# Kernel tuning notes

Hardware: AMD Instinct MI355X
Metric: run time of the kernel (lower is better)

## Reference

```python
import jax, jax.numpy as jnp
import numpy as np

N, E, IN, HID, OUT = 40000, 640000, 128, 512, 256


def setup_inputs() -> dict:
    key = jax.random.key(0)
    ks = jax.random.split(key, 8)
    x = jax.random.normal(ks[0], (N, IN), dtype=jnp.float32)
    edge_index = jax.random.randint(ks[1], (2, E), 0, N, dtype=jnp.int64)
    # SAGEConv params: lin_l (applied to aggregated neighbors, with bias),
    # lin_r (applied to root nodes, no bias) -- PyG defaults.
    def lin(k, fin, fout):
        return jax.random.normal(k, (fin, fout), dtype=jnp.float32) / np.sqrt(fin)
    return {
        "x": x,
        "edge_index": edge_index,
        "W1l": lin(ks[2], IN, HID),
        "b1": jnp.zeros((HID,), jnp.float32),
        "W1r": lin(ks[3], IN, HID),
        "W2l": lin(ks[4], HID, OUT),
        "b2": jnp.zeros((OUT,), jnp.float32),
        "W2r": lin(ks[5], HID, OUT),
    }


def _sage_conv(x, src, dst, Wl, b, Wr):
    n = x.shape[0]
    # gather messages from source nodes, mean-aggregate at destination
    msg = x[src]                                            # [E, F]
    agg = jax.ops.segment_sum(msg, dst, num_segments=n)     # [N, F]
    cnt = jax.ops.segment_sum(jnp.ones((src.shape[0],), x.dtype), dst,
                              num_segments=n)               # [N]
    agg = agg / jnp.maximum(cnt, 1.0)[:, None]
    # out = lin_l(mean_neighbors) + lin_r(x)
    return agg @ Wl + b + x @ Wr


def reference(x, edge_index, W1l, b1, W1r, W2l, b2, W2r):
    src, dst = edge_index[0], edge_index[1]
    h = jax.nn.relu(_sage_conv(x, src, dst, W1l, b1, W1r))
    return _sage_conv(h, src, dst, W2l, b2, W2r)
```

## Files before the change

### kernel.cpp

```cpp
#include <hip/hip_runtime.h>


#define N_NODES 40000
#define N_EDGES 640000
#define F_IN 128
#define F_HID 512
#define F_OUT 256
#define NB_SCAN 157

typedef unsigned short ushort_t;
typedef __attribute__((ext_vector_type(8))) short bf16x8;
typedef __attribute__((ext_vector_type(4))) float floatx4;

__device__ __forceinline__ ushort_t f2bf(float f) {
  union { float f; unsigned int u; } x; x.f = f;
  unsigned int r = (x.u + 0x7FFFu + ((x.u >> 16) & 1u)) >> 16;
  return (ushort_t)r;
}
__device__ __forceinline__ float bf2f(ushort_t u) {
  union { unsigned int u; float f; } x; x.u = ((unsigned int)u) << 16;
  return x.f;
}

__global__ void deg_kernel(const int* __restrict__ ei, int* __restrict__ deg) {
  int e = blockIdx.x * blockDim.x + threadIdx.x;
  if (e < N_EDGES) atomicAdd(&deg[ei[N_EDGES + e]], 1);
}

__global__ void scanA_kernel(const int* __restrict__ deg, int* __restrict__ bsum) {
  __shared__ int sdata[256];
  int i = blockIdx.x * 256 + threadIdx.x;
  sdata[threadIdx.x] = (i < N_NODES) ? deg[i] : 0;
  __syncthreads();
  #pragma unroll
  for (int off = 128; off > 0; off >>= 1) {
    if (threadIdx.x < off) sdata[threadIdx.x] += sdata[threadIdx.x + off];
    __syncthreads();
  }
  if (threadIdx.x == 0) bsum[blockIdx.x] = sdata[0];
}

__global__ void scanB_kernel(const int* __restrict__ bsum, int* __restrict__ boff) {
  __shared__ int buf[2][256];
  int tid = threadIdx.x;
  int v = (tid < NB_SCAN) ? bsum[tid] : 0;
  buf[0][tid] = v;
  __syncthreads();
  int cur = 0;
  #pragma unroll
  for (int off = 1; off < 256; off <<= 1) {
    int val = buf[cur][tid];
    if (tid >= off) val += buf[cur][tid - off];
    buf[cur ^ 1][tid] = val;
    __syncthreads();
    cur ^= 1;
  }
  if (tid < NB_SCAN) boff[tid] = buf[cur][tid] - v;
}

__global__ void scanC_kernel(const int* __restrict__ deg, const int* __restrict__ boff,
                             int* __restrict__ rowptr, int* __restrict__ cursor) {
  __shared__ int buf[2][256];
  int tid = threadIdx.x;
  int i = blockIdx.x * 256 + tid;
  int v = (i < N_NODES) ? deg[i] : 0;
  buf[0][tid] = v;
  __syncthreads();
  int cur = 0;
  #pragma unroll
  for (int off = 1; off < 256; off <<= 1) {
    int val = buf[cur][tid];
    if (tid >= off) val += buf[cur][tid - off];
    buf[cur ^ 1][tid] = val;
    __syncthreads();
    cur ^= 1;
  }
  if (i < N_NODES) {
    int ex = boff[blockIdx.x] + buf[cur][tid] - v;
    rowptr[i] = ex;
    cursor[i] = ex;
    if (i == N_NODES - 1) rowptr[N_NODES] = ex + v;
  }
}

__global__ void fill_kernel(const int* __restrict__ ei, int* __restrict__ cursor,
                            int* __restrict__ col) {
  int e = blockIdx.x * blockDim.x + threadIdx.x;
  if (e < N_EDGES) {
    int d = ei[N_EDGES + e];
    int s = ei[e];
    int pos = atomicAdd(&cursor[d], 1);
    col[pos] = s;
  }
}

__global__ void cvt_x_kernel(const float* __restrict__ x, ushort_t* __restrict__ xb) {
  int i = blockIdx.x * blockDim.x + threadIdx.x;
  const int n4 = (N_NODES * F_IN) / 4;
  if (i < n4) {
    float4 v = ((const float4*)x)[i];
    ushort4 o;
    o.x = f2bf(v.x); o.y = f2bf(v.y); o.z = f2bf(v.z); o.w = f2bf(v.w);
    ((ushort4*)xb)[i] = o;
  }
}

__global__ void wp_kernel(const float* __restrict__ W, ushort_t* __restrict__ Wp,
                          int K, int N, int rowoff, int koff, int KT) {
  int i = blockIdx.x * blockDim.x + threadIdx.x;
  if (i < K * N) {
    int n = i / K, k = i - n * K;
    int ng = rowoff + n, kg = koff + k;
    int gg = ng >> 6, ni = (ng >> 4) & 3, lm = ng & 15;
    int c = kg >> 3, j = kg & 7, t = c >> 2, qk = c & 3;
    size_t dst = (((size_t)(gg * (KT / 32) + t) * 4 + ni) * 64 + qk * 16 + lm) * 8 + j;
    Wp[dst] = f2bf(W[(size_t)k * N + n]);
  }
}

__global__ void biascat_kernel(const float* __restrict__ b2, float* __restrict__ bc) {
  int i = threadIdx.x + blockIdx.x * blockDim.x;
  if (i < 512) bc[i] = (i < 256) ? 0.f : b2[i - 256];
}

__global__ void agg1_kernel(const ushort_t* __restrict__ Xb, ushort_t* __restrict__ Yb,
                            const int* __restrict__ rowptr, const int* __restrict__ colidx) {
  __shared__ int cols[64];
  int n = blockIdx.x, f = threadIdx.x;
  int s = rowptr[n], e = rowptr[n + 1];
  float s0 = 0.f, s1 = 0.f;
  for (int base = s; base < e; base += 64) {
    int cnt = min(64, e - base);
    __syncthreads();
    if (f < cnt) cols[f] = colidx[base + f];
    __syncthreads();
    int j = 0;
    for (; j + 8 <= cnt; j += 8) {
      unsigned int v[8];
      #pragma unroll
      for (int u = 0; u < 8; ++u)
        v[u] = *(const unsigned int*)(Xb + (size_t)cols[j + u] * F_IN + 2 * f);
      #pragma unroll
      for (int u = 0; u < 8; ++u) {
        s0 += bf2f((ushort_t)(v[u] & 0xffffu));
        s1 += bf2f((ushort_t)(v[u] >> 16));
      }
    }
    for (; j < cnt; ++j) {
      unsigned int v = *(const unsigned int*)(Xb + (size_t)cols[j] * F_IN + 2 * f);
      s0 += bf2f((ushort_t)(v & 0xffffu));
      s1 += bf2f((ushort_t)(v >> 16));
    }
  }
  float inv = 1.f / fmaxf((float)(e - s), 1.f);
  unsigned int o = (unsigned int)f2bf(s0 * inv) | ((unsigned int)f2bf(s1 * inv) << 16);
  *(unsigned int*)(Yb + (size_t)n * F_IN + 2 * f) = o;
}

__global__ void agg2_kernel(const ushort_t* __restrict__ hl, const float* __restrict__ hr,
                            float* __restrict__ out,
                            const int* __restrict__ rowptr, const int* __restrict__ colidx) {
  __shared__ int cols[128];
  int n = blockIdx.x, f = threadIdx.x;
  int s = rowptr[n], e = rowptr[n + 1];
  float2 hrv = *(const float2*)(hr + (size_t)n * F_OUT + 2 * f);
  float s0 = 0.f, s1 = 0.f;
  for (int base = s; base < e; base += 128) {
    int cnt = min(128, e - base);
    __syncthreads();
    if (f < cnt) cols[f] = colidx[base + f];
    __syncthreads();
    int j = 0;
    for (; j + 8 <= cnt; j += 8) {
      unsigned int v[8];
      #pragma unroll
      for (int u = 0; u < 8; ++u)
        v[u] = *(const unsigned int*)(hl + (size_t)cols[j + u] * F_OUT + 2 * f);
      #pragma unroll
      for (int u = 0; u < 8; ++u) {
        s0 += bf2f((ushort_t)(v[u] & 0xffffu));
        s1 += bf2f((ushort_t)(v[u] >> 16));
      }
    }
    for (; j < cnt; ++j) {
      unsigned int v = *(const unsigned int*)(hl + (size_t)cols[j] * F_OUT + 2 * f);
      s0 += bf2f((ushort_t)(v & 0xffffu));
      s1 += bf2f((ushort_t)(v >> 16));
    }
  }
  float inv = 1.f / fmaxf((float)(e - s), 1.f);
  float2 o;
  o.x = s0 * inv + hrv.x;
  o.y = s1 * inv + hrv.y;
  *(float2*)(out + (size_t)n * F_OUT + 2 * f) = o;
}

template <bool TWOPAIR, bool RELU, bool BIAS, bool OUT_BF16, bool SPLITOUT, int KT>
__global__ __launch_bounds__(256) void gemm_mfma(
    const ushort_t* __restrict__ A0, const ushort_t* __restrict__ A1,
    const ushort_t* __restrict__ Wp, const float* __restrict__ bias,
    float* __restrict__ Cf, ushort_t* __restrict__ Cb, int M) {
  const int KH = (KT > 256) ? 256 : KT;
  const int NH = KT / KH;
  const int NKH = KH / 8;
  __shared__ ushort_t Apan[64 * KH];
  const int tid = threadIdx.x;
  const int wave = tid >> 6, lane = tid & 63;
  const int lm = lane & 15, qk = lane >> 4;
  const int bn = blockIdx.x * 256;
  const int bm = blockIdx.y * 64;
  const int K0 = TWOPAIR ? KT / 2 : KT;
  const int K0c = K0 / 8;

  const ushort_t* wpg = Wp + (size_t)(blockIdx.x * 4 + wave) * (KT / 32) * 2048;

  auto stageA = [&](int h) {
    #pragma unroll
    for (int q = 0; q < (64 * NKH) / 256; ++q) {
      int c = tid + q * 256;
      int lc = c & (NKH - 1);
      int row = c / NKH;
      int kc = h * NKH + lc;
      const ushort_t* src = (TWOPAIR && kc >= K0c)
          ? A1 + (size_t)(bm + row) * K0 + (kc - K0c) * 8
          : A0 + (size_t)(bm + row) * K0 + kc * 8;
      bf16x8 v = *(const bf16x8*)src;
      size_t off = ((size_t)(lc * 64 + row) * 16) ^ (size_t)((lc & 7) << 4);
      *(bf16x8*)((char*)Apan + off) = v;
    }
  };

  stageA(0);
  bf16x8 bvA[4], bvB[4];
  #pragma unroll
  for (int ni = 0; ni < 4; ++ni)
    bvA[ni] = *(const bf16x8*)(wpg + (size_t)ni * 512 + lane * 8);
  __syncthreads();

  floatx4 acc[4][4] = {};
  #pragma unroll 1
  for (int h = 0; h < NH; ++h) {
    if (h) {
      __syncthreads();
      stageA(h);
      __syncthreads();
    }
    #pragma unroll 1
    for (int kb = 0; kb < KH; kb += 64) {
      const int t0 = (h * KH + kb) / 32;
      #pragma unroll
      for (int ni = 0; ni < 4; ++ni)
        bvB[ni] = *(const bf16x8*)(wpg + ((size_t)(t0 + 1) * 4 + ni) * 512 + lane * 8);

      bf16x8 av[4];
      const int kc0 = kb / 8 + qk;
      #pragma unroll
      for (int mi = 0; mi < 4; ++mi) {
        size_t off = ((size_t)(kc0 * 64 + mi * 16 + lm) * 16) ^ (size_t)((kc0 & 7) << 4);
        av[mi] = *(const bf16x8*)((char*)Apan + off);
      }
      #pragma unroll
      for (int mi = 0; mi < 4; ++mi)
        #pragma unroll
        for (int ni = 0; ni < 4; ++ni)
          acc[mi][ni] = __builtin_amdgcn_mfma_f32_16x16x32_bf16(
              bvA[ni], av[mi], acc[mi][ni], 0, 0, 0);

      if (h * KH + kb + 64 < KT) {
        #pragma unroll
        for (int ni = 0; ni < 4; ++ni)
          bvA[ni] = *(const bf16x8*)(wpg + ((size_t)(t0 + 2) * 4 + ni) * 512 + lane * 8);
      }

      const int kc1 = kb / 8 + 4 + qk;
      #pragma unroll
      for (int mi = 0; mi < 4; ++mi) {
        size_t off = ((size_t)(kc1 * 64 + mi * 16 + lm) * 16) ^ (size_t)((kc1 & 7) << 4);
        av[mi] = *(const bf16x8*)((char*)Apan + off);
      }
      #pragma unroll
      for (int mi = 0; mi < 4; ++mi)
        #pragma unroll
        for (int ni = 0; ni < 4; ++ni)
          acc[mi][ni] = __builtin_amdgcn_mfma_f32_16x16x32_bf16(
              bvB[ni], av[mi], acc[mi][ni], 0, 0, 0);
    }
  }

  #pragma unroll
  for (int ni = 0; ni < 4; ++ni) {
    int colg = bn + wave * 64 + ni * 16 + qk * 4;
    float4 b4 = {0.f, 0.f, 0.f, 0.f};
    if (BIAS) b4 = *(const float4*)&bias[colg];
    #pragma unroll
    for (int mi = 0; mi < 4; ++mi) {
      int rowg = bm + mi * 16 + lm;
      float v0 = acc[mi][ni][0] + b4.x;
      float v1 = acc[mi][ni][1] + b4.y;
      float v2 = acc[mi][ni][2] + b4.z;
      float v3 = acc[mi][ni][3] + b4.w;
      if (RELU) {
        v0 = fmaxf(v0, 0.f); v1 = fmaxf(v1, 0.f);
        v2 = fmaxf(v2, 0.f); v3 = fmaxf(v3, 0.f);
      }
      if (SPLITOUT) {
        if (colg < 256) {
          ushort4 o = {f2bf(v0), f2bf(v1), f2bf(v2), f2bf(v3)};
          *(ushort4*)&Cb[(size_t)rowg * 256 + colg] = o;
        } else {
          float4 o = {v0, v1, v2, v3};
          *(float4*)&Cf[(size_t)rowg * 256 + (colg - 256)] = o;
        }
      } else if (OUT_BF16) {
        ushort4 o = {f2bf(v0), f2bf(v1), f2bf(v2), f2bf(v3)};
        *(ushort4*)&Cb[(size_t)rowg * 512 + colg] = o;
      } else {
        float4 o = {v0, v1, v2, v3};
        *(float4*)&Cf[(size_t)rowg * 512 + colg] = o;
      }
    }
  }
}

extern "C" void kernel_launch(void* const* d_in, const int* in_sizes, int n_in,
                              void* d_out, int out_size, void* d_ws, size_t ws_size,
                              hipStream_t stream) {
  const float* x = (const float*)d_in[0];
  const int* ei = (const int*)d_in[1];
  const float* W1l = (const float*)d_in[2];
  const float* b1 = (const float*)d_in[3];
  const float* W1r = (const float*)d_in[4];
  const float* W2l = (const float*)d_in[5];
  const float* b2 = (const float*)d_in[6];
  const float* W2r = (const float*)d_in[7];
  float* out = (float*)d_out;

  char* ws = (char*)d_ws;
  size_t off = 0;
  auto alloc = [&](size_t bytes) {
    void* p = ws + off;
    off = (off + bytes + 255) & ~(size_t)255;
    return p;
  };
  int* deg = (int*)alloc((size_t)N_NODES * 4);
  int* rowptr = (int*)alloc((size_t)(N_NODES + 1) * 4);
  int* cursor = (int*)alloc((size_t)N_NODES * 4);
  int* col = (int*)alloc((size_t)N_EDGES * 4);
  int* bsum = (int*)alloc((size_t)NB_SCAN * 4);
  int* boff = (int*)alloc((size_t)NB_SCAN * 4);
  ushort_t* x_bf = (ushort_t*)alloc((size_t)N_NODES * F_IN * 2);
  ushort_t* aggx_bf = (ushort_t*)alloc((size_t)N_NODES * F_IN * 2);
  ushort_t* h_bf = (ushort_t*)alloc((size_t)N_NODES * F_HID * 2);
  ushort_t* hl_bf = (ushort_t*)alloc((size_t)N_NODES * F_OUT * 2);
  float* hr = (float*)alloc((size_t)N_NODES * F_OUT * 4);
  ushort_t* Wp1 = (ushort_t*)alloc((size_t)512 * 256 * 2);
  ushort_t* Wp2 = (ushort_t*)alloc((size_t)512 * 512 * 2);
  float* biascat = (float*)alloc(512 * 4);

  hipMemsetAsync(deg, 0, (size_t)N_NODES * 4, stream);
  deg_kernel<<<(N_EDGES + 255) / 256, 256, 0, stream>>>(ei, deg);
  scanA_kernel<<<NB_SCAN, 256, 0, stream>>>(deg, bsum);
  scanB_kernel<<<1, 256, 0, stream>>>(bsum, boff);
  scanC_kernel<<<NB_SCAN, 256, 0, stream>>>(deg, boff, rowptr, cursor);
  fill_kernel<<<(N_EDGES + 255) / 256, 256, 0, stream>>>(ei, cursor, col);

  cvt_x_kernel<<<(N_NODES * F_IN / 4 + 255) / 256, 256, 0, stream>>>(x, x_bf);
  wp_kernel<<<(F_IN * F_HID + 255) / 256, 256, 0, stream>>>(W1l, Wp1, 128, 512, 0, 0, 256);
  wp_kernel<<<(F_IN * F_HID + 255) / 256, 256, 0, stream>>>(W1r, Wp1, 128, 512, 0, 128, 256);
  wp_kernel<<<(F_HID * F_OUT + 255) / 256, 256, 0, stream>>>(W2l, Wp2, 512, 256, 0, 0, 512);
  wp_kernel<<<(F_HID * F_OUT + 255) / 256, 256, 0, stream>>>(W2r, Wp2, 512, 256, 256, 0, 512);
  biascat_kernel<<<2, 256, 0, stream>>>(b2, biascat);

  agg1_kernel<<<N_NODES, 64, 0, stream>>>(x_bf, aggx_bf, rowptr, col);
  gemm_mfma<true, true, true, true, false, 256>
      <<<dim3(2, N_NODES / 64), 256, 0, stream>>>(
          aggx_bf, x_bf, Wp1, b1, nullptr, h_bf, N_NODES);

  gemm_mfma<false, false, true, false, true, 512>
      <<<dim3(2, N_NODES / 64), 256, 0, stream>>>(
          h_bf, nullptr, Wp2, biascat, hr, hl_bf, N_NODES);
  agg2_kernel<<<N_NODES, 128, 0, stream>>>(hl_bf, hr, out, rowptr, col);
}
```

Baseline: 306.8 us.

## Merge prep kernels into one launch and widen GEMM blocks to full N

Folds the x conversion, four weight-packing launches, bias concat and degree counting into a single prep kernel, with block-index ranges picking the task, to cut launch overhead. The GEMM now uses 512-thread blocks of eight waves that cover all 512 output columns for a 64-row tile, so each A panel is staged into shared memory once instead of twice across two column blocks. The grid drops to 625 blocks, which lowers parallelism and may reduce occupancy because of the larger blocks.

New measurement: 297.6 us. 3.0% less time.

```diff
diff --git a/kernel.cpp b/kernel.cpp
--- a/kernel.cpp
+++ b/kernel.cpp
@@ -20,11 +20,6 @@
 __device__ __forceinline__ float bf2f(ushort_t u) {
   union { unsigned int u; float f; } x; x.u = ((unsigned int)u) << 16;
   return x.f;
-}
-
-__global__ void deg_kernel(const int* __restrict__ ei, int* __restrict__ deg) {
-  int e = blockIdx.x * blockDim.x + threadIdx.x;
-  if (e < N_EDGES) atomicAdd(&deg[ei[N_EDGES + e]], 1);
 }
 
 __global__ void scanA_kernel(const int* __restrict__ deg, int* __restrict__ bsum) {
@@ -94,20 +89,10 @@
   }
 }
 
-__global__ void cvt_x_kernel(const float* __restrict__ x, ushort_t* __restrict__ xb) {
-  int i = blockIdx.x * blockDim.x + threadIdx.x;
-  const int n4 = (N_NODES * F_IN) / 4;
-  if (i < n4) {
-    float4 v = ((const float4*)x)[i];
-    ushort4 o;
-    o.x = f2bf(v.x); o.y = f2bf(v.y); o.z = f2bf(v.z); o.w = f2bf(v.w);
-    ((ushort4*)xb)[i] = o;
-  }
-}
-
-__global__ void wp_kernel(const float* __restrict__ W, ushort_t* __restrict__ Wp,
-                          int K, int N, int rowoff, int koff, int KT) {
-  int i = blockIdx.x * blockDim.x + threadIdx.x;
+__device__ __forceinline__ void wp_body(const float* __restrict__ W,
+                                        ushort_t* __restrict__ Wp,
+                                        int i, int K, int N, int rowoff, int koff,
+                                        int KT) {
   if (i < K * N) {
     int n = i / K, k = i - n * K;
     int ng = rowoff + n, kg = koff + k;
@@ -118,9 +103,38 @@
   }
 }
 
-__global__ void biascat_kernel(const float* __restrict__ b2, float* __restrict__ bc) {
-  int i = threadIdx.x + blockIdx.x * blockDim.x;
-  if (i < 512) bc[i] = (i < 256) ? 0.f : b2[i - 256];
+#define PREP_BLOCKS 9038
+__global__ void prep_kernel(const float* __restrict__ x, ushort_t* __restrict__ xb,
+                            const float* __restrict__ W1l, const float* __restrict__ W1r,
+                            const float* __restrict__ W2l, const float* __restrict__ W2r,
+                            ushort_t* __restrict__ Wp1, ushort_t* __restrict__ Wp2,
+                            const float* __restrict__ b2, float* __restrict__ bc,
+                            const int* __restrict__ ei, int* __restrict__ deg) {
+  int b = blockIdx.x, tid = threadIdx.x;
+  if (b < 5000) {
+    int i = b * 256 + tid;
+    const int n4 = (N_NODES * F_IN) / 4;
+    if (i < n4) {
+      float4 v = ((const float4*)x)[i];
+      ushort4 o;
+      o.x = f2bf(v.x); o.y = f2bf(v.y); o.z = f2bf(v.z); o.w = f2bf(v.w);
+      ((ushort4*)xb)[i] = o;
+    }
+  } else if (b < 5256) {
+    wp_body(W1l, Wp1, (b - 5000) * 256 + tid, 128, 512, 0, 0, 256);
+  } else if (b < 5512) {
+    wp_body(W1r, Wp1, (b - 5256) * 256 + tid, 128, 512, 0, 128, 256);
+  } else if (b < 6024) {
+    wp_body(W2l, Wp2, (b - 5512) * 256 + tid, 512, 256, 0, 0, 512);
+  } else if (b < 6536) {
+    wp_body(W2r, Wp2, (b - 6024) * 256 + tid, 512, 256, 256, 0, 512);
+  } else if (b < 6538) {
+    int i = (b - 6536) * 256 + tid;
+    if (i < 512) bc[i] = (i < 256) ? 0.f : b2[i - 256];
+  } else {
+    int e = (b - 6538) * 256 + tid;
+    if (e < N_EDGES) atomicAdd(&deg[ei[N_EDGES + e]], 1);
+  }
 }
 
 __global__ void agg1_kernel(const ushort_t* __restrict__ Xb, ushort_t* __restrict__ Yb,
@@ -196,7 +210,7 @@
 }
 
 template <bool TWOPAIR, bool RELU, bool BIAS, bool OUT_BF16, bool SPLITOUT, int KT>
-__global__ __launch_bounds__(256) void gemm_mfma(
+__global__ __launch_bounds__(512) void gemm_mfma(
     const ushort_t* __restrict__ A0, const ushort_t* __restrict__ A1,
     const ushort_t* __restrict__ Wp, const float* __restrict__ bias,
     float* __restrict__ Cf, ushort_t* __restrict__ Cb, int M) {
@@ -207,17 +221,16 @@
   const int tid = threadIdx.x;
   const int wave = tid >> 6, lane = tid & 63;
   const int lm = lane & 15, qk = lane >> 4;
-  const int bn = blockIdx.x * 256;
-  const int bm = blockIdx.y * 64;
+  const int bm = blockIdx.x * 64;
   const int K0 = TWOPAIR ? KT / 2 : KT;
   const int K0c = K0 / 8;
 
-  const ushort_t* wpg = Wp + (size_t)(blockIdx.x * 4 + wave) * (KT / 32) * 2048;
+  const ushort_t* wpg = Wp + (size_t)wave * (KT / 32) * 2048;
 
   auto stageA = [&](int h) {
     #pragma unroll
-    for (int q = 0; q < (64 * NKH) / 256; ++q) {
-      int c = tid + q * 256;
+    for (int q = 0; q < (64 * NKH) / 512; ++q) {
+      int c = tid + q * 512;
       int lc = c & (NKH - 1);
       int row = c / NKH;
       int kc = h * NKH + lc;
@@ -289,7 +302,7 @@
 
   #pragma unroll
   for (int ni = 0; ni < 4; ++ni) {
-    int colg = bn + wave * 64 + ni * 16 + qk * 4;
+    int colg = wave * 64 + ni * 16 + qk * 4;
     float4 b4 = {0.f, 0.f, 0.f, 0.f};
     if (BIAS) b4 = *(const float4*)&bias[colg];
     #pragma unroll
@@ -358,26 +371,21 @@
   float* biascat = (float*)alloc(512 * 4);
 
   hipMemsetAsync(deg, 0, (size_t)N_NODES * 4, stream);
-  deg_kernel<<<(N_EDGES + 255) / 256, 256, 0, stream>>>(ei, deg);
+  prep_kernel<<<PREP_BLOCKS, 256, 0, stream>>>(
+      x, x_bf, W1l, W1r, W2l, W2r, Wp1, Wp2, b2, biascat, ei, deg);
+
   scanA_kernel<<<NB_SCAN, 256, 0, stream>>>(deg, bsum);
   scanB_kernel<<<1, 256, 0, stream>>>(bsum, boff);
   scanC_kernel<<<NB_SCAN, 256, 0, stream>>>(deg, boff, rowptr, cursor);
   fill_kernel<<<(N_EDGES + 255) / 256, 256, 0, stream>>>(ei, cursor, col);
 
-  cvt_x_kernel<<<(N_NODES * F_IN / 4 + 255) / 256, 256, 0, stream>>>(x, x_bf);
-  wp_kernel<<<(F_IN * F_HID + 255) / 256, 256, 0, stream>>>(W1l, Wp1, 128, 512, 0, 0, 256);
-  wp_kernel<<<(F_IN * F_HID + 255) / 256, 256, 0, stream>>>(W1r, Wp1, 128, 512, 0, 128, 256);
-  wp_kernel<<<(F_HID * F_OUT + 255) / 256, 256, 0, stream>>>(W2l, Wp2, 512, 256, 0, 0, 512);
-  wp_kernel<<<(F_HID * F_OUT + 255) / 256, 256, 0, stream>>>(W2r, Wp2, 512, 256, 256, 0, 512);
-  biascat_kernel<<<2, 256, 0, stream>>>(b2, biascat);
-
   agg1_kernel<<<N_NODES, 64, 0, stream>>>(x_bf, aggx_bf, rowptr, col);
   gemm_mfma<true, true, true, true, false, 256>
-      <<<dim3(2, N_NODES / 64), 256, 0, stream>>>(
+      <<<625, 512, 0, stream>>>(
           aggx_bf, x_bf, Wp1, b1, nullptr, h_bf, N_NODES);
 
   gemm_mfma<false, false, true, false, true, 512>
-      <<<dim3(2, N_NODES / 64), 256, 0, stream>>>(
+      <<<625, 512, 0, stream>>>(
           h_bf, nullptr, Wp2, biascat, hr, hl_bf, N_NODES);
   agg2_kernel<<<N_NODES, 128, 0, stream>>>(hl_bf, hr, out, rowptr, col);
 }
```
